# Kernel optimization log

Measured on AMD Instinct MI355X. Metric: run time of the kernel, lower is better.

Reference implementation:

```python
import jax, jax.numpy as jnp
import numpy as np

B, S, D = 4, 512, 2048
N_HEADS, N_KV, HEAD_DIM = 16, 4, 128
N_REP = N_HEADS // N_KV
FFN = 5632
E, TOPK, R = 8, 2, 16
LORA_SCALE = 32.0 / R  # alpha / r
EPS = 1e-5


def setup_inputs() -> dict:
    key = jax.random.key(0)
    ks = jax.random.split(key, 32)

    def p(k, shape, s=0.02):
        return jax.random.normal(k, shape, jnp.float32) * s

    data = jax.random.normal(ks[0], (B, S, D), jnp.float32)
    # causal additive mask [1,1,S,S]
    causal = jnp.tril(jnp.ones((S, S), jnp.bool_))
    mask = jnp.where(causal, 0.0, -1e9).astype(jnp.float32)[None, None]
    # rotary angles (llama interleaved pairing), half head_dim
    inv_freq = 1.0 / (10000.0 ** (np.arange(0, HEAD_DIM, 2, dtype=np.float32) / HEAD_DIM))
    angles = jnp.asarray(np.arange(S, dtype=np.float32)[:, None] * inv_freq[None, :])
    rope_cos = jnp.cos(angles)  # [S, HEAD_DIM//2]
    rope_sin = jnp.sin(angles)

    inp = dict(
        data=data, mask=mask, rope_cos=rope_cos, rope_sin=rope_sin,
        att_norm_w=jnp.ones((D,), jnp.float32),
        ffn_norm_w=jnp.ones((D,), jnp.float32),
        wq=p(ks[1], (D, D)), wk=p(ks[2], (N_KV * HEAD_DIM, D)),
        wv=p(ks[3], (N_KV * HEAD_DIM, D)), wo=p(ks[4], (D, D)),
        lqA=p(ks[5], (R, D)), lqB=p(ks[6], (D, R)),
        lkA=p(ks[7], (R, D)), lkB=p(ks[8], (N_KV * HEAD_DIM, R)),
        lvA=p(ks[9], (R, D)), lvB=p(ks[10], (N_KV * HEAD_DIM, R)),
        loA=p(ks[11], (R, D)), loB=p(ks[12], (D, R)),
        w1=p(ks[13], (FFN, D)), w2=p(ks[14], (D, FFN)), w3=p(ks[15], (FFN, D)),
        gate_w=p(ks[16], (E, D)),
        eA1=p(ks[17], (E, R, D)), eB1=p(ks[18], (E, FFN, R)),
        eA2=p(ks[19], (E, R, FFN)), eB2=p(ks[20], (E, D, R)),
        eA3=p(ks[21], (E, R, D)), eB3=p(ks[22], (E, FFN, R)),
    )
    return inp


def rmsnorm(x, w):
    return x * jax.lax.rsqrt(jnp.mean(x * x, axis=-1, keepdims=True) + EPS) * w


def lora_linear(x, W, A, Bm):
    # torch Linear weight is [out, in]; lora: x @ A^T @ B^T * scale
    return x @ W.T + ((x @ A.T) @ Bm.T) * LORA_SCALE


def apply_rope(x, cos, sin):
    # x: [B,S,H,Dh]; interleaved complex rotation per pair
    x1, x2 = x[..., 0::2], x[..., 1::2]
    c = cos[None, :, None, :]
    s = sin[None, :, None, :]
    o1 = x1 * c - x2 * s
    o2 = x1 * s + x2 * c
    return jnp.stack([o1, o2], axis=-1).reshape(x.shape)


def transformer_fwd(data, mask, rope_cos, rope_sin, att_norm_w, ffn_norm_w,
                    wq, wk, wv, wo, lqA, lqB, lkA, lkB, lvA, lvB, loA, loB,
                    w1, w2, w3, gate_w, eA1, eB1, eA2, eB2, eA3, eB3):
    b, s, _ = data.shape
    h = rmsnorm(data, att_norm_w)
    xq = lora_linear(h, wq, lqA, lqB).reshape(b, s, N_HEADS, HEAD_DIM)
    xk = lora_linear(h, wk, lkA, lkB).reshape(b, s, N_KV, HEAD_DIM)
    xv = lora_linear(h, wv, lvA, lvB).reshape(b, s, N_KV, HEAD_DIM)
    xq = apply_rope(xq, rope_cos, rope_sin)
    xk = apply_rope(xk, rope_cos, rope_sin)
    # repeat_kv: each kv head repeated n_rep times consecutively
    xk = jnp.repeat(xk, N_REP, axis=2)
    xv = jnp.repeat(xv, N_REP, axis=2)
    scores = jnp.einsum('bshd,bthd->bhst', xq, xk) / jnp.sqrt(jnp.float32(HEAD_DIM))
    scores = scores + mask
    attn = jax.nn.softmax(scores, axis=-1)
    out = jnp.einsum('bhst,bthd->bshd', attn, xv).reshape(b, s, D)
    data = data + lora_linear(out, wo, loA, loB)

    # MoE FFN (MixLoRA): shared base w1/w2/w3 + per-expert LoRA, top-k routing
    hn = rmsnorm(data, ffn_norm_w)
    x = hn.reshape(b * s, D)
    logits = x @ gate_w.T                       # [T, E]
    probs = jax.nn.softmax(logits, axis=-1)
    vals, idx = jax.lax.top_k(probs, TOPK)      # [T, k]
    vals = vals / jnp.sum(vals, axis=-1, keepdims=True)
    T = b * s
    route = jnp.zeros((T, E), x.dtype).at[jnp.arange(T)[:, None], idx].set(vals)
    h1 = x @ w1.T   # shared base projections
    h3 = x @ w3.T
    acc = jnp.zeros((T, D), x.dtype)
    for e in range(E):
        g1 = h1 + ((x @ eA1[e].T) @ eB1[e].T) * LORA_SCALE
        g3 = h3 + ((x @ eA3[e].T) @ eB3[e].T) * LORA_SCALE
        gh = jax.nn.silu(g1) * g3
        oe = gh @ w2.T + ((gh @ eA2[e].T) @ eB2[e].T) * LORA_SCALE
        acc = acc + route[:, e:e + 1] * oe
    return data + acc.reshape(b, s, D)


def reference(data, mask, rope_cos, rope_sin, att_norm_w, ffn_norm_w,
              wq, wk, wv, wo, lqA, lqB, lkA, lkB, lvA, lvB, loA, loB,
              w1, w2, w3, gate_w, eA1, eB1, eA2, eB2, eA3, eB3):
    return transformer_fwd(data, mask, rope_cos, rope_sin, att_norm_w, ffn_norm_w,
                           wq, wk, wv, wo, lqA, lqB, lkA, lkB, lvA, lvB, loA, loB,
                           w1, w2, w3, gate_w, eA1, eB1, eA2, eB2, eA3, eB3)
```

## Files before the change

### kernel.cpp

```cpp
#include <hip/hip_runtime.h>
#include <stdint.h>

#define DI static __device__ __forceinline__

typedef __attribute__((ext_vector_type(8))) short bf16x8;
typedef __attribute__((ext_vector_type(4))) float floatx4;

DI unsigned short f2bf(float x){
  unsigned int u = __float_as_uint(x);
  u += 0x7fffu + ((u >> 16) & 1u);
  return (unsigned short)(u >> 16);
}
DI float bf2f(unsigned short h){ return __uint_as_float(((unsigned int)h) << 16); }

#define GLOAD16(gp, lp) \
  __builtin_amdgcn_global_load_lds((const __attribute__((address_space(1))) unsigned int*)(gp), \
                                   (__attribute__((address_space(3))) unsigned int*)(lp), 16, 0, 0)

#define WAITVM(n) asm volatile("s_waitcnt vmcnt(" #n ")" ::: "memory")

template<int OUTM, int RESM, bool CSKIP, bool SPLIT>
__global__ __launch_bounds__(256, 2)
void k_gemm(const unsigned short* __restrict__ A, long lda, long sA1, long sA2, long aLo,
            const unsigned short* __restrict__ B, long ldb, long sB1, long sB2, long bLo,
            void* __restrict__ C, long ldc, long sC1, long sC2, long cLo,
            const void* __restrict__ Rz, long ldr,
            const unsigned short* __restrict__ G1p, const float* __restrict__ ewp, int slot,
            int kIters, int zshift, int bshift)
{
  if (CSKIP && blockIdx.y > blockIdx.x) return;
  __shared__ __attribute__((aligned(16))) unsigned short As[SPLIT ? 8192 : 4096];
  __shared__ __attribute__((aligned(16))) unsigned short Bs[SPLIT ? 8192 : 4096];
  const int tid = threadIdx.x;
  const int w = tid >> 6, lane = tid & 63;
  const int wm = (w >> 1) * 64, wn = (w & 1) * 64;
  const int z = blockIdx.z;
  const int zr = z & ((1 << zshift) - 1);
  const int zb = z >> zshift;
  long k0 = 0;
  if (OUTM == 2 || OUTM == 8) k0 = (long)zb * (long)kIters * 32;
  const unsigned short* Ab = A + (long)((OUTM==8)?0:zb) * sA2 + (long)zr * sA1 + (long)blockIdx.x * 128 * lda + k0;
  const unsigned short* Bb = B + (long)((OUTM==8)?0:zb) * sB2 + (long)(zr >> bshift) * sB1 + (long)blockIdx.y * 128 * ldb + k0;

  const int rlo = w * 16 + (lane & 15);
  const int rhi = 64 + rlo;
  const int cc  = (lane >> 4) * 8;
  unsigned short* ldsA0 = As + w * 512;
  unsigned short* ldsA1 = As + 2048 + w * 512;
  unsigned short* ldsB0 = Bs + w * 512;
  unsigned short* ldsB1 = Bs + 2048 + w * 512;

  floatx4 acc[4][4];
  floatx4 zv = {0.f, 0.f, 0.f, 0.f};
#pragma unroll
  for (int i = 0; i < 4; ++i)
#pragma unroll
    for (int j = 0; j < 4; ++j) acc[i][j] = zv;

  const int abase = (wm >> 4) * 512 + lane * 8;
  const int bbase = (wn >> 4) * 512 + lane * 8;

  for (int kt = 0; kt < kIters; ++kt) {
    const unsigned short* pa = Ab + (long)kt * 32;
    const unsigned short* pb = Bb + (long)kt * 32;
    GLOAD16(pa + (long)rlo * lda + cc, ldsA0);
    GLOAD16(pa + (long)rhi * lda + cc, ldsA1);
    GLOAD16(pb + (long)rlo * ldb + cc, ldsB0);
    GLOAD16(pb + (long)rhi * ldb + cc, ldsB1);
    if (SPLIT) {
      const unsigned short* pal = pa + aLo;
      const unsigned short* pbl = pb + bLo;
      GLOAD16(pal + (long)rlo * lda + cc, As + 4096 + w * 512);
      GLOAD16(pal + (long)rhi * lda + cc, As + 6144 + w * 512);
      GLOAD16(pbl + (long)rlo * ldb + cc, Bs + 4096 + w * 512);
      GLOAD16(pbl + (long)rhi * ldb + cc, Bs + 6144 + w * 512);
    }
    __syncthreads();
    bf16x8 af[4], bfr[4];
#pragma unroll
    for (int i = 0; i < 4; ++i)
      af[i] = *(const bf16x8*)(As + abase + i * 512);
#pragma unroll
    for (int j = 0; j < 4; ++j)
      bfr[j] = *(const bf16x8*)(Bs + bbase + j * 512);
    if (SPLIT) {
      bf16x8 al[4], bl[4];
#pragma unroll
      for (int i = 0; i < 4; ++i)
        al[i] = *(const bf16x8*)(As + 4096 + abase + i * 512);
#pragma unroll
      for (int j = 0; j < 4; ++j)
        bl[j] = *(const bf16x8*)(Bs + 4096 + bbase + j * 512);
#pragma unroll
      for (int i = 0; i < 4; ++i)
#pragma unroll
        for (int j = 0; j < 4; ++j) {
          acc[i][j] = __builtin_amdgcn_mfma_f32_16x16x32_bf16(af[i], bfr[j], acc[i][j], 0, 0, 0);
          acc[i][j] = __builtin_amdgcn_mfma_f32_16x16x32_bf16(af[i], bl[j], acc[i][j], 0, 0, 0);
          acc[i][j] = __builtin_amdgcn_mfma_f32_16x16x32_bf16(al[i], bfr[j], acc[i][j], 0, 0, 0);
        }
    } else {
#pragma unroll
      for (int i = 0; i < 4; ++i)
#pragma unroll
        for (int j = 0; j < 4; ++j)
          acc[i][j] = __builtin_amdgcn_mfma_f32_16x16x32_bf16(af[i], bfr[j], acc[i][j], 0, 0, 0);
    }
    __syncthreads();
  }

  const long mb = (long)blockIdx.x * 128 + wm + ((lane >> 4) * 4);
  const long nb = (long)blockIdx.y * 128 + wn + (lane & 15);
  const long cbase = (long)zb * sC2 + (long)zr * sC1;
#pragma unroll
  for (int i = 0; i < 4; ++i) {
#pragma unroll
    for (int j = 0; j < 4; ++j) {
#pragma unroll
      for (int rr = 0; rr < 4; ++rr) {
        long m = mb + i * 16 + rr;
        long n = nb + j * 16;
        float v = acc[i][j][rr];
        if (RESM == 1) v += ((const float*)Rz)[m * ldr + n];
        if (RESM == 2) v += bf2f(((const unsigned short*)Rz)[m * ldr + n]);
        if (OUTM == 0 || OUTM == 8) ((float*)C)[cbase + m * ldc + n] = v;
        else if (OUTM == 1) ((unsigned short*)C)[cbase + m * ldc + n] = f2bf(v);
        else if (OUTM == 2) atomicAdd((float*)C + cbase + m * ldc + n, v);
        else if (OUTM == 4) {
          float g1 = bf2f(G1p[m * ldc + n]);
          float s1 = g1 / (1.f + __expf(-g1));
          ((unsigned short*)C)[cbase + m * ldc + n] = f2bf(ewp[m * 2 + slot] * s1 * v);
        } else if (OUTM == 5) {
          unsigned short h = f2bf(v);
          unsigned short l = f2bf(v - bf2f(h));
          ((unsigned short*)C)[cbase + m * ldc + n] = h;
          ((unsigned short*)C)[cbase + m * ldc + n + cLo] = l;
        } else {
          long bq = m >> 9, sI = m & 511, kv = n >> 7, dI = n & 127;
          long t = (((bq * 4 + kv) * 128 + dI) << 9) + sI;
          unsigned short h = f2bf(v);
          unsigned short l = f2bf(v - bf2f(h));
          ((unsigned short*)C)[t] = h;
          ((unsigned short*)C)[t + cLo] = l;
        }
      }
    }
  }
}

template<int BM, int BN, bool SPLIT, int OUTM, int DEPTH>
__global__ __launch_bounds__(512, 2)
void k_gemm2(const unsigned short* __restrict__ A, long lda, long aLo,
             const unsigned short* __restrict__ B, long ldb, long bLo,
             void* __restrict__ C, long ldc, long sC2, int kIters)
{
  constexpr int ASZ = BM * 32 * (SPLIT ? 2 : 1);
  constexpr int BSZ = BN * 32 * (SPLIT ? 2 : 1);
  constexpr int TSZ = ASZ + BSZ;
  constexpr int FM = BM / 32, FN = BN / 64;
  constexpr int LPT = (SPLIT ? 2 : 1) * (BM / 128 + BN / 128);
  static_assert(LPT == 3 || LPT == 4 || LPT == 6 || LPT == 8, "vmcnt literals");
  __shared__ __attribute__((aligned(16))) unsigned short sm[DEPTH * TSZ];

  const int tid = threadIdx.x;
  const int w = tid >> 6, lane = tid & 63;
  const int wm = (w >> 2) * (BM / 2), wn = (w & 3) * (BN / 4);
  const int zb = blockIdx.z;
  const long k0 = (OUTM == 8) ? (long)zb * (long)kIters * 32 : 0;
  const unsigned short* Ab = A + (long)blockIdx.x * BM * lda + k0;
  const unsigned short* Bb = B + (long)blockIdx.y * BN * ldb + k0;
  const int rA = lane & 15;
  const int cc = (lane >> 4) * 8;

  floatx4 acc[FM][FN];
  floatx4 zv = {0.f, 0.f, 0.f, 0.f};
#pragma unroll
  for (int i = 0; i < FM; ++i)
#pragma unroll
    for (int j = 0; j < FN; ++j) acc[i][j] = zv;

  auto stage = [&](int kt, int sl) {
    const unsigned short* pa = Ab + (long)kt * 32;
    const unsigned short* pb = Bb + (long)kt * 32;
    unsigned short* sa = sm + (size_t)sl * TSZ;
    unsigned short* sb = sa + ASZ;
#pragma unroll
    for (int r = 0; r < BM / 128; ++r) {
      const int b = r * 8 + w;
      const long row = b * 16 + rA;
      GLOAD16(pa + row * lda + cc, sa + b * 512);
      if (SPLIT) GLOAD16(pa + aLo + row * lda + cc, sa + BM * 32 + b * 512);
    }
#pragma unroll
    for (int r = 0; r < BN / 128; ++r) {
      const int b = r * 8 + w;
      const long row = b * 16 + rA;
      GLOAD16(pb + row * ldb + cc, sb + b * 512);
      if (SPLIT) GLOAD16(pb + bLo + row * ldb + cc, sb + BN * 32 + b * 512);
    }
  };

  auto waitpipe = [&](int ahead) {
    if (ahead <= 0) { WAITVM(0); return; }
    if (LPT == 3) { if (ahead == 1) { WAITVM(3); } else { WAITVM(6); } }
    else if (LPT == 4) { if (ahead == 1) { WAITVM(4); } else { WAITVM(8); } }
    else if (LPT == 6) { if (ahead == 1) { WAITVM(6); } else { WAITVM(12); } }
    else { if (ahead == 1) { WAITVM(8); } else { WAITVM(16); } }
  };

  int np = DEPTH - 1; if (np > kIters) np = kIters;
  for (int p = 0; p < np; ++p) stage(p, p);
  __builtin_amdgcn_sched_barrier(0);
  waitpipe(np - 1);
  __builtin_amdgcn_s_barrier();

  const int aoff = (wm >> 4) * 512 + lane * 8;
  const int boff = (wn >> 4) * 512 + lane * 8;

  int cs = 0;
  int ss = (np < DEPTH) ? np : 0;
  for (int kt = 0; kt < kIters; ++kt) {
    if (kt + DEPTH - 1 < kIters) {
      stage(kt + DEPTH - 1, ss);
      ss = (ss + 1 == DEPTH) ? 0 : ss + 1;
    }

    const unsigned short* sa = sm + (size_t)cs * TSZ;
    const unsigned short* sb = sa + ASZ;
    if (SPLIT) {
      bf16x8 bfr[FN], bl[FN];
#pragma unroll
      for (int j = 0; j < FN; ++j) {
        bfr[j] = *(const bf16x8*)(sb + boff + j * 512);
        bl[j]  = *(const bf16x8*)(sb + BN * 32 + boff + j * 512);
      }
      __builtin_amdgcn_s_setprio(1);
#pragma unroll
      for (int i = 0; i < FM; ++i) {
        bf16x8 ai = *(const bf16x8*)(sa + aoff + i * 512);
        bf16x8 ali = *(const bf16x8*)(sa + BM * 32 + aoff + i * 512);
#pragma unroll
        for (int j = 0; j < FN; ++j) {
          acc[i][j] = __builtin_amdgcn_mfma_f32_16x16x32_bf16(ai, bfr[j], acc[i][j], 0, 0, 0);
          acc[i][j] = __builtin_amdgcn_mfma_f32_16x16x32_bf16(ai, bl[j], acc[i][j], 0, 0, 0);
          acc[i][j] = __builtin_amdgcn_mfma_f32_16x16x32_bf16(ali, bfr[j], acc[i][j], 0, 0, 0);
        }
      }
      __builtin_amdgcn_s_setprio(0);
    } else {
      bf16x8 bfr[FN];
#pragma unroll
      for (int j = 0; j < FN; ++j)
        bfr[j] = *(const bf16x8*)(sb + boff + j * 512);
      __builtin_amdgcn_s_setprio(1);
#pragma unroll
      for (int i = 0; i < FM; ++i) {
        bf16x8 ai = *(const bf16x8*)(sa + aoff + i * 512);
#pragma unroll
        for (int j = 0; j < FN; ++j)
          acc[i][j] = __builtin_amdgcn_mfma_f32_16x16x32_bf16(ai, bfr[j], acc[i][j], 0, 0, 0);
      }
      __builtin_amdgcn_s_setprio(0);
    }

    __builtin_amdgcn_sched_barrier(0);
    int ahead = kIters - 2 - kt;
    if (ahead > DEPTH - 2) ahead = DEPTH - 2;
    if (ahead < 0) ahead = 0;
    waitpipe(ahead);
    __builtin_amdgcn_s_barrier();
    cs = (cs + 1 == DEPTH) ? 0 : cs + 1;
  }

  const long mb = (long)blockIdx.x * BM + wm + ((lane >> 4) * 4);
  const long nb = (long)blockIdx.y * BN + wn + (lane & 15);
  const long cbase = (long)zb * sC2;
#pragma unroll
  for (int i = 0; i < FM; ++i) {
#pragma unroll
    for (int j = 0; j < FN; ++j) {
#pragma unroll
      for (int rr = 0; rr < 4; ++rr) {
        long m = mb + i * 16 + rr;
        long n = nb + j * 16;
        float v = acc[i][j][rr];
        if (OUTM == 8) ((float*)C)[cbase + m * ldc + n] = v;
        else ((unsigned short*)C)[m * ldc + n] = f2bf(v);
      }
    }
  }
}

__global__ void k_rmsnorm(const float* __restrict__ x, const float* __restrict__ w,
                          unsigned short* __restrict__ ob, long loOff){
  int t = blockIdx.x;
  const float* row = x + (size_t)t * 2048;
  float ss = 0.f;
  for (int i = threadIdx.x; i < 2048; i += 256){ float v = row[i]; ss += v * v; }
#pragma unroll
  for (int o = 32; o; o >>= 1) ss += __shfl_xor(ss, o);
  __shared__ float sred[4]; __shared__ float srms;
  int lane = threadIdx.x & 63, wid = threadIdx.x >> 6;
  if (lane == 0) sred[wid] = ss;
  __syncthreads();
  if (threadIdx.x == 0) srms = rsqrtf((sred[0]+sred[1]+sred[2]+sred[3]) * (1.f/2048.f) + 1e-5f);
  __syncthreads();
  float rr = srms;
  for (int i = threadIdx.x; i < 2048; i += 256){
    float v = row[i] * rr * w[i];
    unsigned short h = f2bf(v);
    ob[(size_t)t * 2048 + i] = h;
    if (loOff) ob[(size_t)t * 2048 + i + loOff] = f2bf(v - bf2f(h));
  }
}

__global__ void k_fold(const float* __restrict__ W, const float* __restrict__ Bm,
                       const float* __restrict__ A, unsigned short* __restrict__ out, long loOff){
  int idx = blockIdx.x * 256 + threadIdx.x;
  int n = idx >> 11, k = idx & 2047;
  float acc = W[idx];
  const float* br = Bm + (size_t)n * 16;
#pragma unroll
  for (int r = 0; r < 16; ++r) acc += 2.0f * br[r] * A[r * 2048 + k];
  unsigned short h = f2bf(acc);
  out[idx] = h;
  out[idx + loOff] = f2bf(acc - bf2f(h));
}

__global__ void k_cvt4(const float* __restrict__ in, unsigned short* __restrict__ out){
  int i = (blockIdx.x * 256 + threadIdx.x) * 4;
  float4 v = *(const float4*)(in + i);
  unsigned long long pk = (unsigned long long)f2bf(v.x)
    | ((unsigned long long)f2bf(v.y) << 16)
    | ((unsigned long long)f2bf(v.z) << 32)
    | ((unsigned long long)f2bf(v.w) << 48);
  *(unsigned long long*)(out + i) = pk;
}

__global__ void k_beff(const float* __restrict__ eB, unsigned short* __restrict__ out, int F){
  int idx = blockIdx.x * 256 + threadIdx.x;
  int f = idx >> 7, er = idx & 127;
  int e = er >> 4, r = er & 15;
  out[idx] = f2bf(eB[((size_t)e * F + f) * 16 + r]);
}

__global__ void k_qkv_epi(const float* __restrict__ P,
                          const float* __restrict__ rc, const float* __restrict__ rs,
                          unsigned short* __restrict__ qb, unsigned short* __restrict__ kb,
                          unsigned short* __restrict__ vT){
  int idx = blockIdx.x * 256 + threadIdx.x;
  int t = idx / 1536, p = idx - t * 1536;
  int c = p * 2;
  const float2 a = *(const float2*)(P + (size_t)t * 3072 + c);
  const float2 b = *(const float2*)(P + 6291456 + (size_t)t * 3072 + c);
  float v0 = a.x + b.x, v1 = a.y + b.y;
  int s = t & 511;
  if (c < 2560) {
    int i = (c & 127) >> 1;
    float co = rc[s * 64 + i], sn = rs[s * 64 + i];
    float o0 = v0 * co - v1 * sn;
    float o1 = v0 * sn + v1 * co;
    v0 = o0; v1 = o1;
  }
  unsigned short h0 = f2bf(v0), l0 = f2bf(v0 - bf2f(h0));
  unsigned short h1 = f2bf(v1), l1 = f2bf(v1 - bf2f(h1));
  if (c < 2048) {
    size_t o = (size_t)t * 2048 + c;
    qb[o] = h0; qb[o + 1] = h1;
    qb[o + 4194304] = l0; qb[o + 4194305] = l1;
  } else if (c < 2560) {
    size_t o = (size_t)t * 512 + (c - 2048);
    kb[o] = h0; kb[o + 1] = h1;
    kb[o + 1048576] = l0; kb[o + 1048577] = l1;
  } else {
    int d = c - 2560;
    int kv = d >> 7, dI = d & 127, bq = t >> 9;
    size_t o = (((size_t)(bq * 4 + kv) * 128 + dI) << 9) + s;
    vT[o] = h0; vT[o + 512] = h1;
    vT[o + 1048576] = l0; vT[o + 1048576 + 512] = l1;
  }
}

__global__ void k_add2res(const float* __restrict__ P, const float* __restrict__ res,
                          float* __restrict__ out){
  int i = (blockIdx.x * 256 + threadIdx.x) * 4;
  float4 a = *(const float4*)(P + i);
  float4 b = *(const float4*)(P + 4194304 + i);
  float4 r = *(const float4*)(res + i);
  float4 o; o.x = a.x + b.x + r.x; o.y = a.y + b.y + r.y;
  o.z = a.z + b.z + r.z; o.w = a.w + b.w + r.w;
  *(float4*)(out + i) = o;
}

__global__ void k_softmax(float* __restrict__ sp){
  int row = blockIdx.x;
  int s = row & 511;
  float* in = sp + (size_t)row * 512;
  unsigned short* op = (unsigned short*)in;
  int t0 = threadIdx.x, t1 = threadIdx.x + 256;
  const float scale = 0.088388347648318447f;
  float v0 = (t0 <= s) ? in[t0] * scale : -3.0e38f;
  float v1 = (t1 <= s) ? in[t1] * scale : -3.0e38f;
  float mx = fmaxf(v0, v1);
#pragma unroll
  for (int o = 32; o; o >>= 1) mx = fmaxf(mx, __shfl_xor(mx, o));
  __shared__ float sred[8];
  int lane = threadIdx.x & 63, wid = threadIdx.x >> 6;
  if (lane == 0) sred[wid] = mx;
  __syncthreads();
  mx = fmaxf(fmaxf(sred[0], sred[1]), fmaxf(sred[2], sred[3]));
  float e0 = (t0 <= s) ? __expf(v0 - mx) : 0.f;
  float e1 = (t1 <= s) ? __expf(v1 - mx) : 0.f;
  float sum = e0 + e1;
#pragma unroll
  for (int o = 32; o; o >>= 1) sum += __shfl_xor(sum, o);
  if (lane == 0) sred[4 + wid] = sum;
  __syncthreads();
  sum = sred[4] + sred[5] + sred[6] + sred[7];
  float inv = 1.f / sum;
  float p0 = e0 * inv, p1 = e1 * inv;
  unsigned short h0 = f2bf(p0), h1 = f2bf(p1);
  op[t0] = h0; op[512 + t0] = f2bf(p0 - bf2f(h0));
  op[t1] = h1; op[512 + t1] = f2bf(p1 - bf2f(h1));
}

__global__ void k_route(const float* __restrict__ x2, const float* __restrict__ w,
                        const float* __restrict__ gw, int* __restrict__ eidx,
                        float* __restrict__ ew){
  int t = blockIdx.x; int lane = threadIdx.x;
  const float* row = x2 + (size_t)t * 2048;
  float ss = 0.f;
  for (int d = lane; d < 2048; d += 64){ float v = row[d]; ss += v * v; }
#pragma unroll
  for (int o = 32; o; o >>= 1) ss += __shfl_xor(ss, o);
  float rr = rsqrtf(ss * (1.f/2048.f) + 1e-5f);
  float acc[8] = {0,0,0,0,0,0,0,0};
  for (int d = lane; d < 2048; d += 64){
    float xv = row[d] * rr * w[d];
#pragma unroll
    for (int e = 0; e < 8; ++e) acc[e] += xv * gw[e * 2048 + d];
  }
#pragma unroll
  for (int e = 0; e < 8; ++e)
#pragma unroll
    for (int o = 32; o; o >>= 1) acc[e] += __shfl_xor(acc[e], o);
  if (lane == 0){
    int i0 = 0;
#pragma unroll
    for (int e = 1; e < 8; ++e) if (acc[e] > acc[i0]) i0 = e;
    int i1 = -1;
#pragma unroll
    for (int e = 0; e < 8; ++e) if (e != i0 && (i1 < 0 || acc[e] > acc[i1])) i1 = e;
    float p1 = __expf(acc[i1] - acc[i0]);
    float inv = 1.f / (1.f + p1);
    eidx[t * 2 + 0] = i0; eidx[t * 2 + 1] = i1;
    ew[t * 2 + 0] = inv;  ew[t * 2 + 1] = p1 * inv;
  }
}

__global__ void k_zero(float* __restrict__ p){
  p[(size_t)blockIdx.x * 256 + threadIdx.x] = 0.f;
}

__global__ void k_ubuild(const float* __restrict__ U1, const float* __restrict__ U3,
                         const int* __restrict__ eidx,
                         unsigned short* __restrict__ u10, unsigned short* __restrict__ u11,
                         unsigned short* __restrict__ u30, unsigned short* __restrict__ u31){
  int idx = blockIdx.x * 256 + threadIdx.x;
  int t = idx >> 7, j = idx & 127; int e = j >> 4;
  int e0 = eidx[t * 2], e1 = eidx[t * 2 + 1];
  float v1 = U1[idx] * 2.0f, v3 = U3[idx] * 2.0f;
  u10[idx] = (e == e0) ? f2bf(v1) : (unsigned short)0;
  u11[idx] = (e == e1) ? f2bf(v1) : (unsigned short)0;
  u30[idx] = (e == e0) ? f2bf(v3) : (unsigned short)0;
  u31[idx] = (e == e1) ? f2bf(v3) : (unsigned short)0;
}

__global__ void k_addip(unsigned short* __restrict__ a, const unsigned short* __restrict__ b){
  size_t i = (size_t)blockIdx.x * 256 + threadIdx.x;
  a[i] = f2bf(bf2f(a[i]) + bf2f(b[i]));
}

__global__ void k_vhat(const float* __restrict__ U20, const float* __restrict__ U21,
                       const int* __restrict__ eidx, unsigned short* __restrict__ out){
  int idx = blockIdx.x * 256 + threadIdx.x;
  int t = idx >> 7, j = idx & 127; int e = j >> 4;
  int e0 = eidx[t * 2], e1 = eidx[t * 2 + 1];
  float v = 0.f;
  if (e == e0) v = 2.0f * U20[idx];
  else if (e == e1) v = 2.0f * U21[idx];
  out[idx] = f2bf(v);
}

extern "C" void kernel_launch(void* const* d_in, const int* in_sizes, int n_in,
                              void* d_out, int out_size, void* d_ws, size_t ws_size,
                              hipStream_t stream){
  const float* data  = (const float*)d_in[0];
  const float* rcos  = (const float*)d_in[2];
  const float* rsin  = (const float*)d_in[3];
  const float* attw  = (const float*)d_in[4];
  const float* ffnw  = (const float*)d_in[5];
  const float* wq    = (const float*)d_in[6];
  const float* wk    = (const float*)d_in[7];
  const float* wv    = (const float*)d_in[8];
  const float* wo    = (const float*)d_in[9];
  const float* lqA   = (const float*)d_in[10];
  const float* lqB   = (const float*)d_in[11];
  const float* lkA   = (const float*)d_in[12];
  const float* lkB   = (const float*)d_in[13];
  const float* lvA   = (const float*)d_in[14];
  const float* lvB   = (const float*)d_in[15];
  const float* loA   = (const float*)d_in[16];
  const float* loB   = (const float*)d_in[17];
  const float* w1    = (const float*)d_in[18];
  const float* w2    = (const float*)d_in[19];
  const float* w3    = (const float*)d_in[20];
  const float* gatew = (const float*)d_in[21];
  const float* eA1   = (const float*)d_in[22];
  const float* eB1   = (const float*)d_in[23];
  const float* eA2   = (const float*)d_in[24];
  const float* eB2   = (const float*)d_in[25];
  const float* eA3   = (const float*)d_in[26];
  const float* eB3   = (const float*)d_in[27];
  (void)in_sizes; (void)n_in; (void)out_size; (void)ws_size;

  char* base = (char*)d_ws;
  float* data2 = (float*)d_out;

  unsigned short* hb   = (unsigned short*)(base + 0);
  unsigned short* Wqkv = (unsigned short*)(base + 16777216);
  float*          QKVf = (float*)(base + 41943040);
  unsigned short* qb   = (unsigned short*)(base + 92274688);
  unsigned short* kb   = (unsigned short*)(base + 109051904);
  unsigned short* vT   = (unsigned short*)(base + 113246208);
  float*          sc   = (float*)(base + 0);
  unsigned short* scU  = (unsigned short*)(base + 0);
  unsigned short* ao   = (unsigned short*)(base + 67108864);
  unsigned short* Wo   = (unsigned short*)(base + 0);
  float*          Wof  = (float*)(base + 16777216);

  size_t off = 0;
  auto alloc = [&](size_t n)->char*{ char* p = base + off; off = (off + n + 255) & ~(size_t)255; return p; };
  int*   eidx = (int*)alloc(16384);
  float* ew   = (float*)alloc(16384);
  unsigned short* hnb  = (unsigned short*)alloc(8388608);
  unsigned short* h1b  = (unsigned short*)alloc(23068672);
  unsigned short* h3b  = (unsigned short*)alloc(23068672);
  unsigned short* wbuf = (unsigned short*)alloc(23068672);
  unsigned short* gh0  = (unsigned short*)alloc(23068672);
  unsigned short* eA1c = (unsigned short*)alloc(524288);
  unsigned short* eA3c = (unsigned short*)alloc(524288);
  unsigned short* eA2c = (unsigned short*)alloc(1441792);
  unsigned short* Bf1  = (unsigned short*)alloc(1441792);
  unsigned short* Bf3  = (unsigned short*)alloc(1441792);
  unsigned short* Bf2  = (unsigned short*)alloc(524288);
  float* Uz = (float*)alloc(4194304);
  float* U1 = Uz, *U3 = Uz + 262144, *U20 = Uz + 524288, *U21 = Uz + 786432;
  unsigned short* Ut10 = (unsigned short*)alloc(524288);
  unsigned short* Ut11 = (unsigned short*)alloc(524288);
  unsigned short* Ut30 = (unsigned short*)alloc(524288);
  unsigned short* Ut31 = (unsigned short*)alloc(524288);
  unsigned short* vhat = (unsigned short*)alloc(524288);
  unsigned short* gh1  = h1b;
  float*          W2f  = (float*)h1b;

  k_rmsnorm<<<2048, 256, 0, stream>>>(data, attw, hb, 4194304);
  k_fold<<<16384, 256, 0, stream>>>(wq, lqB, lqA, Wqkv, 6291456);
  k_fold<<<4096, 256, 0, stream>>>(wk, lkB, lkA, Wqkv + 4194304, 6291456);
  k_fold<<<4096, 256, 0, stream>>>(wv, lvB, lvA, Wqkv + 5242880, 6291456);

  k_gemm2<256,256,true,8,2><<<dim3(8,12,2), 512, 0, stream>>>(
      hb, 2048, 4194304, Wqkv, 2048, 6291456, QKVf, 3072, 6291456, 32);
  k_qkv_epi<<<12288, 256, 0, stream>>>(QKVf, rcos, rsin, qb, kb, vT);

  k_gemm<0,0,true,true><<<dim3(4,4,64), 256, 0, stream>>>(
      qb, 2048, 128, 1048576, 4194304, kb, 512, 128, 262144, 1048576,
      sc, 512, 262144, 4194304, 0, nullptr,0, nullptr,nullptr,0, 4, 4, 2);
  k_softmax<<<32768, 256, 0, stream>>>(sc);
  k_gemm<5,0,false,true><<<dim3(4,1,64), 256, 0, stream>>>(
      scU, 1024, 524288, 8388608, 512, vT, 512, 65536, 262144, 1048576,
      ao, 2048, 128, 1048576, 4194304, nullptr,0, nullptr,nullptr,0, 16, 4, 2);

  k_fold<<<16384, 256, 0, stream>>>(wo, loB, loA, Wo, 4194304);
  k_gemm2<256,128,true,8,3><<<dim3(8,16,2), 512, 0, stream>>>(
      ao, 2048, 4194304, Wo, 2048, 4194304, Wof, 2048, 4194304, 32);
  k_add2res<<<4096, 256, 0, stream>>>(Wof, data, data2);

  k_rmsnorm<<<2048, 256, 0, stream>>>(data2, ffnw, hnb, 0);
  k_route<<<2048, 64, 0, stream>>>(data2, ffnw, gatew, eidx, ew);

  k_cvt4<<<11264, 256, 0, stream>>>(w1, wbuf);
  k_gemm2<256,256,false,1,4><<<dim3(8,22,1), 512, 0, stream>>>(
      hnb, 2048, 0, wbuf, 2048, 0, h1b, 5632, 0, 64);
  k_cvt4<<<11264, 256, 0, stream>>>(w3, wbuf);
  k_gemm2<256,256,false,1,4><<<dim3(8,22,1), 512, 0, stream>>>(
      hnb, 2048, 0, wbuf, 2048, 0, h3b, 5632, 0, 64);

  k_cvt4<<<256, 256, 0, stream>>>(eA1, eA1c);
  k_cvt4<<<256, 256, 0, stream>>>(eA3, eA3c);
  k_cvt4<<<704, 256, 0, stream>>>(eA2, eA2c);
  k_beff<<<2816, 256, 0, stream>>>(eB1, Bf1, 5632);
  k_beff<<<2816, 256, 0, stream>>>(eB3, Bf3, 5632);
  k_beff<<<1024, 256, 0, stream>>>(eB2, Bf2, 2048);
  k_zero<<<4096, 256, 0, stream>>>(Uz);

  k_gemm<2,0,false,false><<<dim3(16,1,8), 256, 0, stream>>>(
      hnb,2048,0,0,0, eA1c,2048,0,0,0, U1,128,0,0,0, nullptr,0, nullptr,nullptr,0, 8,0,0);
  k_gemm<2,0,false,false><<<dim3(16,1,8), 256, 0, stream>>>(
      hnb,2048,0,0,0, eA3c,2048,0,0,0, U3,128,0,0,0, nullptr,0, nullptr,nullptr,0, 8,0,0);
  k_ubuild<<<1024, 256, 0, stream>>>(U1, U3, eidx, Ut10, Ut11, Ut30, Ut31);

  k_gemm<1,2,false,false><<<dim3(16,44,1), 256, 0, stream>>>(
      Ut10,128,0,0,0, Bf1,128,0,0,0, wbuf,5632,0,0,0, h1b,5632, nullptr,nullptr,0, 4,0,0);
  k_gemm<4,2,false,false><<<dim3(16,44,1), 256, 0, stream>>>(
      Ut30,128,0,0,0, Bf3,128,0,0,0, gh0,5632,0,0,0, h3b,5632, wbuf,ew,0, 4,0,0);
  k_gemm<2,0,false,false><<<dim3(16,1,8), 256, 0, stream>>>(
      gh0,5632,0,0,0, eA2c,5632,0,0,0, U20,128,0,0,0, nullptr,0, nullptr,nullptr,0, 22,0,0);
  k_gemm<1,2,false,false><<<dim3(16,44,1), 256, 0, stream>>>(
      Ut11,128,0,0,0, Bf1,128,0,0,0, wbuf,5632,0,0,0, h1b,5632, nullptr,nullptr,0, 4,0,0);
  k_gemm<4,2,false,false><<<dim3(16,44,1), 256, 0, stream>>>(
      Ut31,128,0,0,0, Bf3,128,0,0,0, gh1,5632,0,0,0, h3b,5632, wbuf,ew,1, 4,0,0);
  k_gemm<2,0,false,false><<<dim3(16,1,8), 256, 0, stream>>>(
      gh1,5632,0,0,0, eA2c,5632,0,0,0, U21,128,0,0,0, nullptr,0, nullptr,nullptr,0, 22,0,0);

  k_addip<<<45056, 256, 0, stream>>>(gh0, gh1);
  k_vhat<<<1024, 256, 0, stream>>>(U20, U21, eidx, vhat);
  k_gemm<2,0,false,false><<<dim3(16,16,1), 256, 0, stream>>>(
      vhat,128,0,0,0, Bf2,128,0,0,0, data2,2048,0,0,0, nullptr,0, nullptr,nullptr,0, 4,0,0);
  k_cvt4<<<11264, 256, 0, stream>>>(w2, wbuf);
  k_gemm2<128,256,false,8,4><<<dim3(16,8,2), 512, 0, stream>>>(
      gh0, 5632, 0, wbuf, 5632, 0, W2f, 2048, 4194304, 88);
  k_add2res<<<4096, 256, 0, stream>>>(W2f, data2, data2);
}
```

Before: 1.028 ms.

## Fuse expert gate/up LoRA GEMMs with SwiGLU and retile QKV projection

Replaces the pair of per-slot GEMMs (one writing the g1 intermediate to a buffer, one reading it back for the SiLU·g3·route epilogue) with a single dual-accumulator kernel. It computes both low-rank products, adds the h1/h3 base projections and applies SwiGLU and the routing weight in registers, so the intermediate never round-trips through global memory. Separately, the QKV projection GEMM switches from 256x256 to 256x192 tiles, giving 256 blocks instead of 192 for better CU coverage. To allow tiles that are not a multiple of 128, the loader now guards rows past the tile edge, which is only valid with the depth-2 drain-to-zero wait. The dual kernel carries two sets of accumulators, raising register pressure, and has no software pipelining of its loads.

```diff
diff --git a/kernel.cpp b/kernel.cpp
--- a/kernel.cpp
+++ b/kernel.cpp
@@ -159,6 +159,8 @@
   constexpr int TSZ = ASZ + BSZ;
   constexpr int FM = BM / 32, FN = BN / 64;
   constexpr int LPT = (SPLIT ? 2 : 1) * (BM / 128 + BN / 128);
+  static_assert((BM % 128 == 0 && BN % 128 == 0) || DEPTH == 2,
+                "non-x128 tiles only with drain-to-0 (per-wave vmcnt)");
   static_assert(LPT == 3 || LPT == 4 || LPT == 6 || LPT == 8, "vmcnt literals");
   __shared__ __attribute__((aligned(16))) unsigned short sm[DEPTH * TSZ];
 
@@ -185,18 +187,22 @@
     unsigned short* sa = sm + (size_t)sl * TSZ;
     unsigned short* sb = sa + ASZ;
 #pragma unroll
-    for (int r = 0; r < BM / 128; ++r) {
+    for (int r = 0; r < (BM + 127) / 128; ++r) {
       const int b = r * 8 + w;
-      const long row = b * 16 + rA;
-      GLOAD16(pa + row * lda + cc, sa + b * 512);
-      if (SPLIT) GLOAD16(pa + aLo + row * lda + cc, sa + BM * 32 + b * 512);
-    }
-#pragma unroll
-    for (int r = 0; r < BN / 128; ++r) {
+      if ((BM & 127) == 0 || b * 16 < BM) {
+        const long row = b * 16 + rA;
+        GLOAD16(pa + row * lda + cc, sa + b * 512);
+        if (SPLIT) GLOAD16(pa + aLo + row * lda + cc, sa + BM * 32 + b * 512);
+      }
+    }
+#pragma unroll
+    for (int r = 0; r < (BN + 127) / 128; ++r) {
       const int b = r * 8 + w;
-      const long row = b * 16 + rA;
-      GLOAD16(pb + row * ldb + cc, sb + b * 512);
-      if (SPLIT) GLOAD16(pb + bLo + row * ldb + cc, sb + BN * 32 + b * 512);
+      if ((BN & 127) == 0 || b * 16 < BN) {
+        const long row = b * 16 + rA;
+        GLOAD16(pb + row * ldb + cc, sb + b * 512);
+        if (SPLIT) GLOAD16(pb + bLo + row * ldb + cc, sb + BN * 32 + b * 512);
+      }
     }
   };
 
@@ -286,6 +292,86 @@
         float v = acc[i][j][rr];
         if (OUTM == 8) ((float*)C)[cbase + m * ldc + n] = v;
         else ((unsigned short*)C)[m * ldc + n] = f2bf(v);
+      }
+    }
+  }
+}
+
+__global__ __launch_bounds__(256, 2)
+void k_gemmdual(const unsigned short* __restrict__ A1, const unsigned short* __restrict__ B1,
+                const unsigned short* __restrict__ A3, const unsigned short* __restrict__ B3,
+                const unsigned short* __restrict__ R1, const unsigned short* __restrict__ R3,
+                unsigned short* __restrict__ C, const float* __restrict__ ewp, int slot)
+{
+  __shared__ __attribute__((aligned(16))) unsigned short A1s[4096];
+  __shared__ __attribute__((aligned(16))) unsigned short A3s[4096];
+  __shared__ __attribute__((aligned(16))) unsigned short B1s[4096];
+  __shared__ __attribute__((aligned(16))) unsigned short B3s[4096];
+  const int tid = threadIdx.x;
+  const int w = tid >> 6, lane = tid & 63;
+  const int wm = (w >> 1) * 64, wn = (w & 1) * 64;
+  const unsigned short* A1b = A1 + (long)blockIdx.x * 128 * 128;
+  const unsigned short* A3b = A3 + (long)blockIdx.x * 128 * 128;
+  const unsigned short* B1b = B1 + (long)blockIdx.y * 128 * 128;
+  const unsigned short* B3b = B3 + (long)blockIdx.y * 128 * 128;
+  const int rlo = w * 16 + (lane & 15);
+  const int rhi = 64 + rlo;
+  const int cc  = (lane >> 4) * 8;
+
+  floatx4 acc1[4][4], acc3[4][4];
+  floatx4 zv = {0.f, 0.f, 0.f, 0.f};
+#pragma unroll
+  for (int i = 0; i < 4; ++i)
+#pragma unroll
+    for (int j = 0; j < 4; ++j) { acc1[i][j] = zv; acc3[i][j] = zv; }
+
+  const int abase = (wm >> 4) * 512 + lane * 8;
+  const int bbase = (wn >> 4) * 512 + lane * 8;
+
+  for (int kt = 0; kt < 4; ++kt) {
+    const long ko = (long)kt * 32;
+    GLOAD16(A1b + (long)rlo * 128 + ko + cc, A1s + w * 512);
+    GLOAD16(A1b + (long)rhi * 128 + ko + cc, A1s + 2048 + w * 512);
+    GLOAD16(A3b + (long)rlo * 128 + ko + cc, A3s + w * 512);
+    GLOAD16(A3b + (long)rhi * 128 + ko + cc, A3s + 2048 + w * 512);
+    GLOAD16(B1b + (long)rlo * 128 + ko + cc, B1s + w * 512);
+    GLOAD16(B1b + (long)rhi * 128 + ko + cc, B1s + 2048 + w * 512);
+    GLOAD16(B3b + (long)rlo * 128 + ko + cc, B3s + w * 512);
+    GLOAD16(B3b + (long)rhi * 128 + ko + cc, B3s + 2048 + w * 512);
+    __syncthreads();
+    bf16x8 b1f[4], b3f[4];
+#pragma unroll
+    for (int j = 0; j < 4; ++j) {
+      b1f[j] = *(const bf16x8*)(B1s + bbase + j * 512);
+      b3f[j] = *(const bf16x8*)(B3s + bbase + j * 512);
+    }
+#pragma unroll
+    for (int i = 0; i < 4; ++i) {
+      bf16x8 a1 = *(const bf16x8*)(A1s + abase + i * 512);
+      bf16x8 a3 = *(const bf16x8*)(A3s + abase + i * 512);
+#pragma unroll
+      for (int j = 0; j < 4; ++j) {
+        acc1[i][j] = __builtin_amdgcn_mfma_f32_16x16x32_bf16(a1, b1f[j], acc1[i][j], 0, 0, 0);
+        acc3[i][j] = __builtin_amdgcn_mfma_f32_16x16x32_bf16(a3, b3f[j], acc3[i][j], 0, 0, 0);
+      }
+    }
+    __syncthreads();
+  }
+
+  const long mb = (long)blockIdx.x * 128 + wm + ((lane >> 4) * 4);
+  const long nb = (long)blockIdx.y * 128 + wn + (lane & 15);
+#pragma unroll
+  for (int i = 0; i < 4; ++i) {
+#pragma unroll
+    for (int j = 0; j < 4; ++j) {
+#pragma unroll
+      for (int rr = 0; rr < 4; ++rr) {
+        long m = mb + i * 16 + rr;
+        long n = nb + j * 16;
+        float g1 = acc1[i][j][rr] + bf2f(R1[m * 5632 + n]);
+        float g3 = acc3[i][j][rr] + bf2f(R3[m * 5632 + n]);
+        float s1 = g1 / (1.f + __expf(-g1));
+        C[m * 5632 + n] = f2bf(ewp[m * 2 + slot] * s1 * g3);
       }
     }
   }
@@ -569,7 +655,7 @@
   k_fold<<<4096, 256, 0, stream>>>(wk, lkB, lkA, Wqkv + 4194304, 6291456);
   k_fold<<<4096, 256, 0, stream>>>(wv, lvB, lvA, Wqkv + 5242880, 6291456);
 
-  k_gemm2<256,256,true,8,2><<<dim3(8,12,2), 512, 0, stream>>>(
+  k_gemm2<256,192,true,8,2><<<dim3(8,16,2), 512, 0, stream>>>(
       hb, 2048, 4194304, Wqkv, 2048, 6291456, QKVf, 3072, 6291456, 32);
   k_qkv_epi<<<12288, 256, 0, stream>>>(QKVf, rcos, rsin, qb, kb, vT);
 
@@ -610,16 +696,12 @@
       hnb,2048,0,0,0, eA3c,2048,0,0,0, U3,128,0,0,0, nullptr,0, nullptr,nullptr,0, 8,0,0);
   k_ubuild<<<1024, 256, 0, stream>>>(U1, U3, eidx, Ut10, Ut11, Ut30, Ut31);
 
-  k_gemm<1,2,false,false><<<dim3(16,44,1), 256, 0, stream>>>(
-      Ut10,128,0,0,0, Bf1,128,0,0,0, wbuf,5632,0,0,0, h1b,5632, nullptr,nullptr,0, 4,0,0);
-  k_gemm<4,2,false,false><<<dim3(16,44,1), 256, 0, stream>>>(
-      Ut30,128,0,0,0, Bf3,128,0,0,0, gh0,5632,0,0,0, h3b,5632, wbuf,ew,0, 4,0,0);
+  k_gemmdual<<<dim3(16,44), 256, 0, stream>>>(
+      Ut10, Bf1, Ut30, Bf3, h1b, h3b, gh0, ew, 0);
   k_gemm<2,0,false,false><<<dim3(16,1,8), 256, 0, stream>>>(
       gh0,5632,0,0,0, eA2c,5632,0,0,0, U20,128,0,0,0, nullptr,0, nullptr,nullptr,0, 22,0,0);
-  k_gemm<1,2,false,false><<<dim3(16,44,1), 256, 0, stream>>>(
-      Ut11,128,0,0,0, Bf1,128,0,0,0, wbuf,5632,0,0,0, h1b,5632, nullptr,nullptr,0, 4,0,0);
-  k_gemm<4,2,false,false><<<dim3(16,44,1), 256, 0, stream>>>(
-      Ut31,128,0,0,0, Bf3,128,0,0,0, gh1,5632,0,0,0, h3b,5632, wbuf,ew,1, 4,0,0);
+  k_gemmdual<<<dim3(16,44), 256, 0, stream>>>(
+      Ut11, Bf1, Ut31, Bf3, h1b, h3b, gh1, ew, 1);
   k_gemm<2,0,false,false><<<dim3(16,1,8), 256, 0, stream>>>(
       gh1,5632,0,0,0, eA2c,5632,0,0,0, U21,128,0,0,0, nullptr,0, nullptr,nullptr,0, 22,0,0);
 
```

Measured after the change: 1.003 ms. 1.02x faster.
